# Optimization experiments

Measured on AMD Instinct MI355X. Metric: run time of the kernel, lower is better.

Reference implementation:

```python
import jax, jax.numpy as jnp
import numpy as np

EMBED_DIM = 1024
NUM_HEADS = 16
D_K = EMBED_DIM // NUM_HEADS


def setup_inputs() -> dict:
    key = jax.random.key(0)
    ks = jax.random.split(key, 5)
    x = jax.random.normal(ks[0], (2, 2048, EMBED_DIM), dtype=jnp.float32)
    # kaiming_normal on 2D params: std = sqrt(2/fan_in) with fan_in = in_features
    w_qkv = jax.random.normal(ks[1], (3 * EMBED_DIM, EMBED_DIM), dtype=jnp.float32) * np.sqrt(2.0 / EMBED_DIM)
    b_qkv = jnp.zeros((3 * EMBED_DIM,), dtype=jnp.float32)
    w_o = jax.random.normal(ks[2], (EMBED_DIM, EMBED_DIM), dtype=jnp.float32) * np.sqrt(2.0 / EMBED_DIM)
    b_o = jnp.zeros((EMBED_DIM,), dtype=jnp.float32)
    return {"x": x, "w_qkv": w_qkv, "b_qkv": b_qkv, "w_o": w_o, "b_o": b_o}


def reference(x, w_qkv, b_qkv, w_o, b_o):
    B, N, C = x.shape
    qkv = x @ w_qkv.T + b_qkv  # [B,N,3C]
    q, k, v = jnp.split(qkv, 3, axis=-1)
    # [B,H,N,d_k]
    q = q.reshape(B, N, NUM_HEADS, D_K).transpose(0, 2, 1, 3)
    k = k.reshape(B, N, NUM_HEADS, D_K).transpose(0, 2, 1, 3)
    v = v.reshape(B, N, NUM_HEADS, D_K).transpose(0, 2, 1, 3)
    # NOTE: original forward scales by 1/sqrt(embed_dim), not 1/sqrt(d_k)
    scores = jnp.einsum('bhqd,bhkd->bhqk', q, k) / np.sqrt(C).astype(np.float32)
    causal = jnp.tril(jnp.ones((N, N), dtype=bool))
    scores = jnp.where(causal, scores, -jnp.inf)
    attn = jax.nn.softmax(scores, axis=-1)
    out = jnp.einsum('bhqk,bhkd->bhqd', attn, v)  # [B,H,N,d_k]
    out = out.transpose(0, 2, 1, 3).reshape(B, N, C)
    return out @ w_o.T + b_o
```

## Files before the change

kernel.cpp:

```cpp
#include <hip/hip_runtime.h>
#include <hip/hip_bf16.h>
#include <math.h>

typedef __bf16 bf16_t;
typedef __bf16 bf16x8 __attribute__((ext_vector_type(8)));
typedef __bf16 bf16x4 __attribute__((ext_vector_type(4)));
typedef __bf16 bf16x2 __attribute__((ext_vector_type(2)));
typedef float f32x4 __attribute__((ext_vector_type(4)));
typedef unsigned u32x4 __attribute__((ext_vector_type(4)));

#define SCALE_L2E 0.045084234f
#define ROUND_B 0.0028169f

#define MFMA16(a, b, c) __builtin_amdgcn_mfma_f32_16x16x32_bf16(a, b, c, 0, 0, 0)

__device__ __forceinline__ unsigned pack2(float a, float b) {
  return __builtin_amdgcn_perm(__builtin_bit_cast(unsigned, b),
                               __builtin_bit_cast(unsigned, a), 0x07060302u);
}

__global__ void convert3_f32_bf16(const float* __restrict__ a, int na,
                                  const float* __restrict__ b, int nb,
                                  const float* __restrict__ c, int nc,
                                  bf16_t* __restrict__ oa, bf16_t* __restrict__ ob,
                                  bf16_t* __restrict__ oc) {
  int i = (blockIdx.x * blockDim.x + threadIdx.x) * 8;
  const float* src;
  bf16_t* dst;
  int off;
  if (i < na) { src = a; dst = oa; off = i; }
  else if (i < na + nb) { src = b; dst = ob; off = i - na; }
  else if (i < na + nb + nc) { src = c; dst = oc; off = i - na - nb; }
  else return;
  float4 u = *(const float4*)&src[off];
  float4 v = *(const float4*)&src[off + 4];
  bf16x8 w = {(bf16_t)u.x, (bf16_t)u.y, (bf16_t)u.z, (bf16_t)u.w,
              (bf16_t)v.x, (bf16_t)v.y, (bf16_t)v.z, (bf16_t)v.w};
  *(bf16x8*)&dst[off] = w;
}

#define GLOBAL_AS __attribute__((address_space(1)))
#define LDS_AS __attribute__((address_space(3)))
__device__ __forceinline__ void g2l16(const void* g, void* l) {
  __builtin_amdgcn_global_load_lds((const GLOBAL_AS void*)g, (LDS_AS void*)l,
                                   16, 0, 0);
}

__launch_bounds__(256, 4)
__global__ void gemm128k32(const bf16_t* __restrict__ A,
                           const bf16_t* __restrict__ B,
                           const float* __restrict__ bias,
                           bf16_t* __restrict__ C,
                           int M, int N, int K) {
  __shared__ __align__(16) bf16_t As[2][128 * 32];
  __shared__ __align__(16) bf16_t Bs[2][128 * 32];

  const int t = threadIdx.x;
  const int wave = t >> 6, lane = t & 63, quad = lane >> 4, ln = lane & 15;
  const int wm = (wave >> 1) * 64, wn = (wave & 1) * 64;
  const int m0 = blockIdx.y * 128, n0 = blockIdx.x * 128;
  const int nt = K >> 5;

  const int srow = lane >> 2;
  const int schunk = ((lane & 3) ^ ((lane >> 3) & 3)) * 8;
  const bf16_t* gA0 = &A[(size_t)(m0 + wave * 32 + srow) * K + schunk];
  const bf16_t* gA1 = gA0 + (size_t)16 * K;
  const bf16_t* gB0 = &B[(size_t)(n0 + wave * 32 + srow) * K + schunk];
  const bf16_t* gB1 = gB0 + (size_t)16 * K;

  const int cslot = (quad ^ ((ln >> 1) & 3)) * 8;

  f32x4 acc[4][4];
#pragma unroll
  for (int i = 0; i < 4; i++)
#pragma unroll
    for (int j = 0; j < 4; j++) acc[i][j] = (f32x4){0.f, 0.f, 0.f, 0.f};

  auto stage = [&](int tl) {
    const int buf = tl & 1;
    const int k0 = tl * 32;
    g2l16(gA0 + k0, &As[buf][(wave * 32) * 32]);
    g2l16(gA1 + k0, &As[buf][(wave * 32 + 16) * 32]);
    g2l16(gB0 + k0, &Bs[buf][(wave * 32) * 32]);
    g2l16(gB1 + k0, &Bs[buf][(wave * 32 + 16) * 32]);
  };

  stage(0);
  __syncthreads();

  for (int tl = 0; tl < nt; ++tl) {
    const int buf = tl & 1;
    if (tl + 1 < nt) stage(tl + 1);
    bf16x8 af[4], bfr[4];
#pragma unroll
    for (int mt = 0; mt < 4; mt++)
      af[mt] = *(const bf16x8*)&As[buf][(wm + mt * 16 + ln) * 32 + cslot];
#pragma unroll
    for (int nf = 0; nf < 4; nf++)
      bfr[nf] = *(const bf16x8*)&Bs[buf][(wn + nf * 16 + ln) * 32 + cslot];
#pragma unroll
    for (int mt = 0; mt < 4; mt++)
#pragma unroll
      for (int nf = 0; nf < 4; nf++)
        acc[mt][nf] = MFMA16(af[mt], bfr[nf], acc[mt][nf]);
    __syncthreads();
  }

#pragma unroll
  for (int nf = 0; nf < 4; nf++) {
    const int col = n0 + wn + nf * 16 + ln;
    const float bv = bias[col];
#pragma unroll
    for (int mt = 0; mt < 4; mt++) {
      const int row = m0 + wm + mt * 16 + quad * 4;
#pragma unroll
      for (int r = 0; r < 4; r++)
        C[(size_t)(row + r) * N + col] = (bf16_t)(acc[mt][nf][r] + bv);
    }
  }
}

template <int BM, typename TC>
__launch_bounds__(256, 2)
__global__ void gemm128db(const bf16_t* __restrict__ A,
                          const bf16_t* __restrict__ B,
                          const float* __restrict__ bias,
                          TC* __restrict__ C,
                          int M, int N, int K) {
  constexpr int MF = BM / 32;
  __shared__ __align__(16) bf16_t Ab[2][BM * 64];
  __shared__ __align__(16) bf16_t Bb[2][128 * 64];

  const int tid = threadIdx.x;
  const int wave = tid >> 6, lane = tid & 63, quad = lane >> 4, ln = lane & 15;
  const int wm = wave >> 1, wn = wave & 1;
  const int m0 = blockIdx.y * BM, n0 = blockIdx.x * 128;
  const int nt = K >> 6;

  const int rowoff = wave * 8 + (lane >> 3);
  const int c8 = ((lane & 7) ^ (lane >> 3)) * 8;
  const int w8row = wave * 8;
  const bf16_t* Arow0 = A + (size_t)(m0 + rowoff) * K + c8;
  const bf16_t* Brow0 = B + (size_t)(n0 + rowoff) * K + c8;

  auto stA = [&](int tl) {
    const bf16_t* g = Arow0 + (size_t)tl * 64;
    bf16_t* l = &Ab[tl & 1][w8row * 64];
#pragma unroll
    for (int rr = 0; rr < BM; rr += 32)
      g2l16(g + (size_t)rr * K, l + rr * 64);
  };
  auto stB = [&](int tl) {
    const bf16_t* g = Brow0 + (size_t)tl * 64;
    bf16_t* l = &Bb[tl & 1][w8row * 64];
#pragma unroll
    for (int rr = 0; rr < 128; rr += 32)
      g2l16(g + (size_t)rr * K, l + rr * 64);
  };

  const int cswl = (quad ^ (ln & 7)) * 8;
  const int aBase = (wm * (BM / 2) + ln) * 64;
  const int bBase = (wn * 64 + ln) * 64;

  f32x4 acc[MF][4];
#pragma unroll
  for (int i = 0; i < MF; i++)
#pragma unroll
    for (int j = 0; j < 4; j++) acc[i][j] = (f32x4){0.f, 0.f, 0.f, 0.f};

  bf16x8 af[MF][2], bfr[4][2];

  auto ldA = [&](int buf) {
#pragma unroll
    for (int mf = 0; mf < MF; ++mf)
#pragma unroll
      for (int sk = 0; sk < 2; ++sk)
        af[mf][sk] = *(const bf16x8*)&Ab[buf][aBase + mf * 1024 +
                                             (cswl ^ (sk << 5))];
  };
  auto ldB = [&](int buf) {
#pragma unroll
    for (int nf = 0; nf < 4; ++nf)
#pragma unroll
      for (int sk = 0; sk < 2; ++sk)
        bfr[nf][sk] = *(const bf16x8*)&Bb[buf][bBase + nf * 1024 +
                                               (cswl ^ (sk << 5))];
  };
  auto mm = [&]() {
#pragma unroll
    for (int mf = 0; mf < MF; ++mf)
#pragma unroll
      for (int nf = 0; nf < 4; ++nf) {
        f32x4 c = acc[mf][nf];
        c = MFMA16(af[mf][0], bfr[nf][0], c);
        c = MFMA16(af[mf][1], bfr[nf][1], c);
        acc[mf][nf] = c;
      }
  };

  stA(0); stB(0);
  __syncthreads();

  for (int tl = 0; tl < nt; ++tl) {
    const int buf = tl & 1;
    if (tl + 1 < nt) { stA(tl + 1); stB(tl + 1); }
    ldA(buf);
    ldB(buf);
    mm();
    __syncthreads();
  }

#pragma unroll
  for (int nf = 0; nf < 4; ++nf) {
    const int col = n0 + wn * 64 + nf * 16 + ln;
    const float bv = bias[col];
#pragma unroll
    for (int mf = 0; mf < MF; ++mf) {
      const int row = m0 + wm * (BM / 2) + mf * 16 + quad * 4;
#pragma unroll
      for (int r = 0; r < 4; ++r)
        C[(size_t)(row + r) * N + col] = (TC)(acc[mf][nf][r] + bv);
    }
  }
}

__launch_bounds__(512, 4)
__global__ void attn_kernel(const bf16_t* __restrict__ qkv,
                            bf16_t* __restrict__ out) {
  constexpr int KP = 72, VP = 72;
  constexpr int BUF = 64 * KP;
  __shared__ __align__(16) bf16_t KsB[2 * BUF];
  __shared__ __align__(16) bf16_t VtB[2 * BUF];

  const int t = threadIdx.x;
  const int wave = t >> 6, lane = t & 63, quad = lane >> 4, ln = lane & 15;
  const int qw = wave & 3;
  const int kh = wave >> 2;
  const int p = blockIdx.x >> 5;
  const int bh = blockIdx.x & 31;
  const int b = bh >> 4, h = bh & 15;
  const int qA = p * 64, qB = (31 - p) * 64;
  const int ntiles = 32 - p;
  const size_t rs = 3072;
  const size_t base = (size_t)b * 2048 * rs;

  const size_t qoffA = base + (size_t)(qA + qw * 16 + ln) * rs + h * 64;
  const size_t qoffB = base + (size_t)(qB + qw * 16 + ln) * rs + h * 64;
  bf16x8 qfA0 = *(const bf16x8*)&qkv[qoffA + quad * 8];
  bf16x8 qfA1 = *(const bf16x8*)&qkv[qoffA + 32 + quad * 8];
  bf16x8 qfB0 = *(const bf16x8*)&qkv[qoffB + quad * 8];
  bf16x8 qfB1 = *(const bf16x8*)&qkv[qoffB + 32 + quad * 8];

  f32x4 oA[4], oB[4];
  f32x4 lAv = (f32x4){0.f, 0.f, 0.f, 0.f};
  f32x4 lBv = (f32x4){0.f, 0.f, 0.f, 0.f};
  for (int ct = 0; ct < 4; ct++) {
    oA[ct] = (f32x4){0.f, 0.f, 0.f, 0.f};
    oB[ct] = (f32x4){0.f, 0.f, 0.f, 0.f};
  }

  const int t256 = t & 255;
  const int r0 = t256 >> 3, c0 = (t256 & 7) * 8;
  const int wav4 = t256 >> 6;
  const int ksA = r0 * KP + (((t256 & 7) + wav4) & 7) * 8;
  const int ksB2 = (r0 + 32) * KP + (((t256 & 7) + wav4 + 4) & 7) * 8;
  const int vkoff = ((((r0 >> 2) + (t256 & 7)) & 7)) * 8 + 2 * (r0 & 3);

  const bf16_t* gp0;
  const bf16_t* gp1;
  if (kh) {
    gp0 = &qkv[base + 1024 + h * 64 + (size_t)r0 * rs + c0];
    gp1 = gp0 + (size_t)32 * rs;
  } else {
    gp0 = &qkv[base + 2048 + h * 64 + (size_t)(2 * r0) * rs + c0];
    gp1 = gp0 + rs;
  }
  const size_t tstep = (size_t)64 * rs;

  bf16x8 s0 = *(const bf16x8*)gp0; gp0 += tstep;
  bf16x8 s1 = *(const bf16x8*)gp1; gp1 += tstep;

  const int qgA = qA + qw * 16 + ln;
  const int qgB = qB + qw * 16 + ln;

  auto stage_to = [&](int buf) {
    if (kh) {
      bf16_t* KsW = &KsB[buf * BUF];
      *(bf16x8*)&KsW[ksA] = s0;
      *(bf16x8*)&KsW[ksB2] = s1;
    } else {
      bf16_t* VtW = &VtB[buf * BUF];
#pragma unroll
      for (int j = 0; j < 8; j++) {
        bf16x2 w2 = {s0[j], s1[j]};
        *(bf16x2*)&VtW[(c0 + j) * VP + vkoff] = w2;
      }
    }
  };
  auto prefetch = [&]() {
    s0 = *(const bf16x8*)gp0; gp0 += tstep;
    s1 = *(const bf16x8*)gp1; gp1 += tstep;
  };
  auto load_kfs = [&](const bf16_t* Ks, bf16x8* kf0s, bf16x8* kf1s) {
#pragma unroll
    for (int sh = 0; sh < 2; sh++) {
      const int st = kh * 2 + sh;
      const int krow = st * 16 + ln;
      const int rot = 2 * st + (ln >> 3);
      kf0s[sh] = *(const bf16x8*)&Ks[krow * KP + ((quad + rot) & 7) * 8];
      kf1s[sh] = *(const bf16x8*)&Ks[krow * KP + ((quad + 4 + rot) & 7) * 8];
    }
  };
  auto qk_block = [&](const bf16x8* kf0s, const bf16x8* kf1s, bf16x8 q0,
                      bf16x8 q1, f32x4& lxv, bf16x8& Bp, bool masked,
                      int kbase, int qg) {
    u32x4 u;
#pragma unroll
    for (int sh = 0; sh < 2; sh++) {
      f32x4 s = (f32x4){0.f, 0.f, 0.f, 0.f};
      __builtin_amdgcn_s_setprio(1);
      s = MFMA16(kf0s[sh], q0, s);
      s = MFMA16(kf1s[sh], q1, s);
      __builtin_amdgcn_s_setprio(0);
      const int k0g = kbase + (kh * 2 + sh) * 16 + quad * 4;
      float pv[4];
#pragma unroll
      for (int r = 0; r < 4; r++) {
        float e = __builtin_amdgcn_exp2f(fmaf(s[r], SCALE_L2E, ROUND_B));
        if (masked && (k0g + r > qg)) e = 0.f;
        lxv[r] += e;
        pv[r] = e;
      }
      u[sh * 2] = pack2(pv[0], pv[1]);
      u[sh * 2 + 1] = pack2(pv[2], pv[3]);
    }
    Bp = __builtin_bit_cast(bf16x8, u);
  };
  auto load_vfs = [&](const bf16_t* Vt, bf16x8* A8s) {
#pragma unroll
    for (int ct = 0; ct < 4; ct++) {
      const int dd = ct * 16 + ln;
      const int bc = (quad >> 1) + 2 * ct + (ln >> 3);
      const int cA = (4 * kh + bc) & 7;
      const int cB = (4 * kh + 2 + bc) & 7;
      bf16x4 v0 = *(const bf16x4*)&Vt[dd * VP + cA * 8 + (quad & 1) * 4];
      bf16x4 v1 = *(const bf16x4*)&Vt[dd * VP + cB * 8 + (quad & 1) * 4];
      A8s[ct] = __builtin_shufflevector(v0, v1, 0, 1, 2, 3, 4, 5, 6, 7);
    }
  };

  auto body = [&](int kt, bool hasA, bool maskA, bool maskB) {
    if (kt + 1 < ntiles) {
      stage_to((kt + 1) & 1);
      if (kt + 2 < ntiles) prefetch();
    }
    const bf16_t* Ks = &KsB[(kt & 1) * BUF];
    const bf16_t* Vt = &VtB[(kt & 1) * BUF];
    bf16x8 kf0s[2], kf1s[2];
    load_kfs(Ks, kf0s, kf1s);
    bf16x8 BpA, BpB;
    if (hasA) qk_block(kf0s, kf1s, qfA0, qfA1, lAv, BpA, maskA, kt * 64, qgA);
    qk_block(kf0s, kf1s, qfB0, qfB1, lBv, BpB, maskB, kt * 64, qgB);
    bf16x8 A8s[4];
    load_vfs(Vt, A8s);
    __builtin_amdgcn_s_setprio(1);
#pragma unroll
    for (int ct = 0; ct < 4; ct++) {
      if (hasA) oA[ct] = MFMA16(A8s[ct], BpA, oA[ct]);
      oB[ct] = MFMA16(A8s[ct], BpB, oB[ct]);
    }
    __builtin_amdgcn_s_setprio(0);
    if (kt + 1 < ntiles) __syncthreads();
  };

  stage_to(0);
  if (ntiles > 1) prefetch();
  __syncthreads();

  for (int kt = 0; kt < p; kt++) body(kt, true, false, false);
  body(p, true, true, false);
  for (int kt = p + 1; kt < 31 - p; kt++) body(kt, false, false, false);
  body(31 - p, false, false, true);

  float lAx = (lAv[0] + lAv[1]) + (lAv[2] + lAv[3]);
  float lBx = (lBv[0] + lBv[1]) + (lBv[2] + lBv[3]);
  lAx += __shfl_xor(lAx, 16);
  lAx += __shfl_xor(lAx, 32);
  lBx += __shfl_xor(lBx, 16);
  lBx += __shfl_xor(lBx, 32);

  __syncthreads();
  float* redA = (float*)KsB;
  float* redB = (float*)VtB;
  const int idx = qw * 64 + lane;
  if (kh) {
#pragma unroll
    for (int ct = 0; ct < 4; ct++) {
      *(f32x4*)&redA[(ct * 256 + idx) * 4] = oA[ct];
      *(f32x4*)&redB[(ct * 256 + idx) * 4] = oB[ct];
    }
    redA[4096 + idx] = lAx;
    redB[4096 + idx] = lBx;
  }
  __syncthreads();
  if (!kh) {
#pragma unroll
    for (int ct = 0; ct < 4; ct++) {
      oA[ct] += *(const f32x4*)&redA[(ct * 256 + idx) * 4];
      oB[ct] += *(const f32x4*)&redB[(ct * 256 + idx) * 4];
    }
    lAx += redA[4096 + idx];
    lBx += redB[4096 + idx];
    const float invA = __builtin_amdgcn_rcpf(lAx);
    const float invB = __builtin_amdgcn_rcpf(lBx);
    const int ocol = h * 64 + quad * 4;
#pragma unroll
    for (int ct = 0; ct < 4; ct++) {
      bf16x4 wa, wb;
#pragma unroll
      for (int r = 0; r < 4; r++) {
        wa[r] = (bf16_t)(oA[ct][r] * invA);
        wb[r] = (bf16_t)(oB[ct][r] * invB);
      }
      *(bf16x4*)&out[(size_t)(b * 2048 + qgA) * 1024 + ocol + ct * 16] = wa;
      *(bf16x4*)&out[(size_t)(b * 2048 + qgB) * 1024 + ocol + ct * 16] = wb;
    }
  }
}

extern "C" void kernel_launch(void* const* d_in, const int* in_sizes, int n_in,
                              void* d_out, int out_size, void* d_ws, size_t ws_size,
                              hipStream_t stream) {
  const float* x     = (const float*)d_in[0];
  const float* w_qkv = (const float*)d_in[1];
  const float* b_qkv = (const float*)d_in[2];
  const float* w_o   = (const float*)d_in[3];
  const float* b_o   = (const float*)d_in[4];
  float* out = (float*)d_out;

  bf16_t* qkv   = (bf16_t*)d_ws;
  bf16_t* xbf   = qkv + (size_t)4096 * 3072;
  bf16_t* wqkvb = xbf + (size_t)4096 * 1024;
  bf16_t* wob   = wqkvb + (size_t)3072 * 1024;
  bf16_t* attn  = xbf;

  const int na = 4096 * 1024, nb = 3072 * 1024, nc = 1024 * 1024;
  convert3_f32_bf16<<<dim3((na + nb + nc) / (256 * 8)), 256, 0, stream>>>(
      x, na, w_qkv, nb, w_o, nc, xbf, wqkvb, wob);

  gemm128k32<<<dim3(3072 / 128, 4096 / 128), 256, 0, stream>>>(
      xbf, wqkvb, b_qkv, qkv, 4096, 3072, 1024);
  attn_kernel<<<dim3(512), 512, 0, stream>>>(qkv, attn);
  gemm128db<64, float><<<dim3(1024 / 128, 4096 / 64), 256, 0, stream>>>(
      attn, wob, b_o, out, 4096, 1024, 1024);
}
```

Baseline: 167.9 us.

## Load K fragments directly from global memory instead of staging through LDS

The K tile is no longer staged into shared memory. Each wave reads its MFMA K fragments straight from global memory at the start of every tile, and only the V transpose still goes through LDS, which is now handled by the kh==0 waves alone. This removes the K LDS writes and reads and halves the LDS buffer footprint, with the reduction scratch remapped onto a single smem array. In exchange the global K loads are issued just before their use with no software prefetch, so their latency may sit on the critical path. Each K row is also fetched by the several waves that share that kh half, which adds redundant global/L2 traffic.

Result: slower. 193.8 us (+15.4%).

```diff
diff --git a/kernel.cpp b/kernel.cpp
--- a/kernel.cpp
+++ b/kernel.cpp
@@ -227,10 +227,10 @@
 __launch_bounds__(512, 4)
 __global__ void attn_kernel(const bf16_t* __restrict__ qkv,
                             bf16_t* __restrict__ out) {
-  constexpr int KP = 72, VP = 72;
-  constexpr int BUF = 64 * KP;
-  __shared__ __align__(16) bf16_t KsB[2 * BUF];
-  __shared__ __align__(16) bf16_t VtB[2 * BUF];
+  constexpr int VP = 72;
+  constexpr int BUF = 64 * VP;
+  __shared__ __align__(16) bf16_t smem[17408];
+  bf16_t* VtB = smem;
 
   const int t = threadIdx.x;
   const int wave = t >> 6, lane = t & 63, quad = lane >> 4, ln = lane & 15;
@@ -259,59 +259,37 @@
     oB[ct] = (f32x4){0.f, 0.f, 0.f, 0.f};
   }
 
+  const bf16_t* kptr = &qkv[base + 1024 + h * 64 +
+                            (size_t)(kh * 32 + ln) * rs + quad * 8];
+  const size_t tstep = (size_t)64 * rs;
+
   const int t256 = t & 255;
   const int r0 = t256 >> 3, c0 = (t256 & 7) * 8;
-  const int wav4 = t256 >> 6;
-  const int ksA = r0 * KP + (((t256 & 7) + wav4) & 7) * 8;
-  const int ksB2 = (r0 + 32) * KP + (((t256 & 7) + wav4 + 4) & 7) * 8;
   const int vkoff = ((((r0 >> 2) + (t256 & 7)) & 7)) * 8 + 2 * (r0 & 3);
-
-  const bf16_t* gp0;
-  const bf16_t* gp1;
-  if (kh) {
-    gp0 = &qkv[base + 1024 + h * 64 + (size_t)r0 * rs + c0];
-    gp1 = gp0 + (size_t)32 * rs;
-  } else {
-    gp0 = &qkv[base + 2048 + h * 64 + (size_t)(2 * r0) * rs + c0];
-    gp1 = gp0 + rs;
-  }
-  const size_t tstep = (size_t)64 * rs;
-
-  bf16x8 s0 = *(const bf16x8*)gp0; gp0 += tstep;
-  bf16x8 s1 = *(const bf16x8*)gp1; gp1 += tstep;
+  const bf16_t* vp0 = &qkv[base + 2048 + h * 64 + (size_t)(2 * r0) * rs + c0];
+  const bf16_t* vp1 = vp0 + rs;
+  bf16x8 s0, s1;
+  if (!kh) {
+    s0 = *(const bf16x8*)vp0; vp0 += tstep;
+    s1 = *(const bf16x8*)vp1; vp1 += tstep;
+  }
 
   const int qgA = qA + qw * 16 + ln;
   const int qgB = qB + qw * 16 + ln;
 
   auto stage_to = [&](int buf) {
-    if (kh) {
-      bf16_t* KsW = &KsB[buf * BUF];
-      *(bf16x8*)&KsW[ksA] = s0;
-      *(bf16x8*)&KsW[ksB2] = s1;
-    } else {
-      bf16_t* VtW = &VtB[buf * BUF];
-#pragma unroll
-      for (int j = 0; j < 8; j++) {
-        bf16x2 w2 = {s0[j], s1[j]};
-        *(bf16x2*)&VtW[(c0 + j) * VP + vkoff] = w2;
-      }
-    }
-  };
-  auto prefetch = [&]() {
-    s0 = *(const bf16x8*)gp0; gp0 += tstep;
-    s1 = *(const bf16x8*)gp1; gp1 += tstep;
-  };
-  auto load_kfs = [&](const bf16_t* Ks, bf16x8* kf0s, bf16x8* kf1s) {
-#pragma unroll
-    for (int sh = 0; sh < 2; sh++) {
-      const int st = kh * 2 + sh;
-      const int krow = st * 16 + ln;
-      const int rot = 2 * st + (ln >> 3);
-      kf0s[sh] = *(const bf16x8*)&Ks[krow * KP + ((quad + rot) & 7) * 8];
-      kf1s[sh] = *(const bf16x8*)&Ks[krow * KP + ((quad + 4 + rot) & 7) * 8];
-    }
-  };
-  auto qk_block = [&](const bf16x8* kf0s, const bf16x8* kf1s, bf16x8 q0,
+    bf16_t* VtW = &VtB[buf * BUF];
+#pragma unroll
+    for (int j = 0; j < 8; j++) {
+      bf16x2 w2 = {s0[j], s1[j]};
+      *(bf16x2*)&VtW[(c0 + j) * VP + vkoff] = w2;
+    }
+  };
+  auto prefetchV = [&]() {
+    s0 = *(const bf16x8*)vp0; vp0 += tstep;
+    s1 = *(const bf16x8*)vp1; vp1 += tstep;
+  };
+  auto qk_block = [&](const bf16x8* k0, const bf16x8* k1, bf16x8 q0,
                       bf16x8 q1, f32x4& lxv, bf16x8& Bp, bool masked,
                       int kbase, int qg) {
     u32x4 u;
@@ -319,8 +297,8 @@
     for (int sh = 0; sh < 2; sh++) {
       f32x4 s = (f32x4){0.f, 0.f, 0.f, 0.f};
       __builtin_amdgcn_s_setprio(1);
-      s = MFMA16(kf0s[sh], q0, s);
-      s = MFMA16(kf1s[sh], q1, s);
+      s = MFMA16(k0[sh], q0, s);
+      s = MFMA16(k1[sh], q1, s);
       __builtin_amdgcn_s_setprio(0);
       const int k0g = kbase + (kh * 2 + sh) * 16 + quad * 4;
       float pv[4];
@@ -350,17 +328,20 @@
   };
 
   auto body = [&](int kt, bool hasA, bool maskA, bool maskB) {
-    if (kt + 1 < ntiles) {
+    bf16x8 k0c[2], k1c[2];
+    k0c[0] = *(const bf16x8*)kptr;
+    k0c[1] = *(const bf16x8*)(kptr + 16 * rs);
+    k1c[0] = *(const bf16x8*)(kptr + 32);
+    k1c[1] = *(const bf16x8*)(kptr + 16 * rs + 32);
+    kptr += tstep;
+    if (!kh && kt + 1 < ntiles) {
       stage_to((kt + 1) & 1);
-      if (kt + 2 < ntiles) prefetch();
-    }
-    const bf16_t* Ks = &KsB[(kt & 1) * BUF];
+      if (kt + 2 < ntiles) prefetchV();
+    }
     const bf16_t* Vt = &VtB[(kt & 1) * BUF];
-    bf16x8 kf0s[2], kf1s[2];
-    load_kfs(Ks, kf0s, kf1s);
     bf16x8 BpA, BpB;
-    if (hasA) qk_block(kf0s, kf1s, qfA0, qfA1, lAv, BpA, maskA, kt * 64, qgA);
-    qk_block(kf0s, kf1s, qfB0, qfB1, lBv, BpB, maskB, kt * 64, qgB);
+    if (hasA) qk_block(k0c, k1c, qfA0, qfA1, lAv, BpA, maskA, kt * 64, qgA);
+    qk_block(k0c, k1c, qfB0, qfB1, lBv, BpB, maskB, kt * 64, qgB);
     bf16x8 A8s[4];
     load_vfs(Vt, A8s);
     __builtin_amdgcn_s_setprio(1);
@@ -373,8 +354,10 @@
     if (kt + 1 < ntiles) __syncthreads();
   };
 
-  stage_to(0);
-  if (ntiles > 1) prefetch();
+  if (!kh) {
+    stage_to(0);
+    if (ntiles > 1) prefetchV();
+  }
   __syncthreads();
 
   for (int kt = 0; kt < p; kt++) body(kt, true, false, false);
@@ -390,8 +373,8 @@
   lBx += __shfl_xor(lBx, 32);
 
   __syncthreads();
-  float* redA = (float*)KsB;
-  float* redB = (float*)VtB;
+  float* redA = (float*)smem;
+  float* redB = (float*)(smem + 8704);
   const int idx = qw * 64 + lane;
   if (kh) {
 #pragma unroll
```
